# Optimization experiments

Measured on AMD Instinct MI355X. Metric: run time of the kernel, lower is better.

Reference implementation:

```python
import jax, jax.numpy as jnp
import numpy as np

N = 50000      # nodes
E = 800000     # edges (before self-loops)
NFEAT = 128
NHID = 32
H = 8
NCLASS = 47
NEG_SLOPE = 0.2  # PyG GATv2Conv default


def gatv2_layer(x, src, dst, Wl, Wr, att, b, n):
    """One GATv2Conv layer (concat over heads). att: [H, C]."""
    h, c = att.shape
    xl = (x @ Wl).reshape(n, h, c)  # source transform (lin_l)
    xr = (x @ Wr).reshape(n, h, c)  # target transform (lin_r)
    e = jax.nn.leaky_relu(xl[src] + xr[dst], NEG_SLOPE)   # [E, H, C]
    logits = jnp.einsum('ehc,hc->eh', e, att)             # [E, H]
    # segment softmax over incoming edges of each target node
    m = jax.ops.segment_max(logits, dst, num_segments=n)  # [N, H]
    alpha = jnp.exp(logits - m[dst])
    denom = jax.ops.segment_sum(alpha, dst, num_segments=n)
    alpha = alpha / (denom[dst] + 1e-16)
    msg = xl[src] * alpha[:, :, None]                     # [E, H, C]
    out = jax.ops.segment_sum(msg, dst, num_segments=n)   # [N, H, C]
    return out.reshape(n, h * c) + b


def setup_inputs():
    key = jax.random.key(0)
    ks = jax.random.split(key, 16)
    s = 0.1
    x = jax.random.normal(ks[0], (N, NFEAT), jnp.float32)
    edge_index = jax.random.randint(ks[1], (2, E), 0, N)
    HID = H * NHID  # 256
    params = dict(
        Wl0=jax.random.normal(ks[2], (NFEAT, HID), jnp.float32) * s,
        Wr0=jax.random.normal(ks[3], (NFEAT, HID), jnp.float32) * s,
        a0=jax.random.normal(ks[4], (H, NHID), jnp.float32) * s,
        b0=jnp.zeros((HID,), jnp.float32),
        Wl1=jax.random.normal(ks[5], (HID, HID), jnp.float32) * s,
        Wr1=jax.random.normal(ks[6], (HID, HID), jnp.float32) * s,
        a1=jax.random.normal(ks[7], (H, NHID), jnp.float32) * s,
        b1=jnp.zeros((HID,), jnp.float32),
        Wl2=jax.random.normal(ks[8], (HID, NCLASS), jnp.float32) * s,
        Wr2=jax.random.normal(ks[9], (HID, NCLASS), jnp.float32) * s,
        a2=jax.random.normal(ks[10], (1, NCLASS), jnp.float32) * s,
        b2=jnp.zeros((NCLASS,), jnp.float32),
    )
    return {"x": x, "edge_index": edge_index, **params}


def reference(x, edge_index, Wl0, Wr0, a0, b0, Wl1, Wr1, a1, b1, Wl2, Wr2, a2, b2):
    n = x.shape[0]
    # PyG GATv2Conv adds self-loops by default
    loops = jnp.arange(n, dtype=edge_index.dtype)
    src = jnp.concatenate([edge_index[0], loops])
    dst = jnp.concatenate([edge_index[1], loops])
    h = gatv2_layer(x, src, dst, Wl0, Wr0, a0, b0, n)
    h = jax.nn.elu(h)
    h = gatv2_layer(h, src, dst, Wl1, Wr1, a1, b1, n)
    h = jax.nn.elu(h)
    h = gatv2_layer(h, src, dst, Wl2, Wr2, a2, b2, n)
    return jax.nn.log_softmax(h, axis=-1)
```

## Files before the change

kernel.cpp:

```cpp
#include <hip/hip_runtime.h>
#include <cmath>


#define NFEAT 128
#define HID 256
#define NCLS 47
#define L2PAD 64
#define LOG2E 1.44269504088896340736f

typedef __attribute__((ext_vector_type(8))) short bf16x8;
typedef __attribute__((ext_vector_type(4))) float f32x4;
typedef __attribute__((ext_vector_type(2))) float f32x2;

__device__ __forceinline__ unsigned short f2b(float f) {
  unsigned int u = __builtin_bit_cast(unsigned int, f);
  u += 0x7FFFu + ((u >> 16) & 1u);
  return (unsigned short)(u >> 16);
}
__device__ __forceinline__ float b2f(unsigned short s) {
  return __builtin_bit_cast(float, (unsigned int)s << 16);
}
__device__ __forceinline__ f32x2 b2f2(unsigned int u) {
  return (f32x2){__builtin_bit_cast(float, u << 16),
                 __builtin_bit_cast(float, u & 0xFFFF0000u)};
}
__device__ __forceinline__ void glds16(const unsigned short* g, unsigned short* l) {
  __builtin_amdgcn_global_load_lds(
      (const __attribute__((address_space(1))) unsigned int*)g,
      (__attribute__((address_space(3))) unsigned int*)l, 16, 0, 0);
}

__global__ void k_cast_bf16(const float* __restrict__ in,
                            unsigned short* __restrict__ out, int n4) {
  int i = blockIdx.x * blockDim.x + threadIdx.x;
  if (i < n4) {
    float4 v = reinterpret_cast<const float4*>(in)[i];
    ushort4 o = {f2b(v.x), f2b(v.y), f2b(v.z), f2b(v.w)};
    reinterpret_cast<ushort4*>(out)[i] = o;
  }
}

struct WtArgs {
  const float* W[6];
  unsigned short* WT[6];
  int K[6], M[6], off[6], total;
  const float* att;
  float* att48;
};
__global__ void k_wt_all(WtArgs a) {
  int i = blockIdx.x * blockDim.x + threadIdx.x;
  if (i >= a.total) {
    int j = i - a.total;
    if (j < 48) a.att48[j] = (j < NCLS) ? a.att[j] * LOG2E : 0.f;
    return;
  }
  int s = 0;
  #pragma unroll
  for (int j = 1; j < 6; ++j) if (i >= a.off[j]) s = j;
  int jj = i - a.off[s];
  int K = a.K[s], M = a.M[s];
  int m = jj / K, k = jj - m * K;
  a.WT[s][jj] = (m < M) ? f2b(a.W[s][(size_t)k * M + m]) : (unsigned short)0;
}

__global__ void k_init_deg(int* __restrict__ deg, int n) {
  int i = blockIdx.x * blockDim.x + threadIdx.x;
  if (i < n) deg[i] = 1;
}

__global__ void k_count(const int* __restrict__ dst, int* __restrict__ deg, int e) {
  int i = blockIdx.x * blockDim.x + threadIdx.x;
  if (i < e) atomicAdd(&deg[dst[i]], 1);
}

__global__ __launch_bounds__(256) void k_bsum(const int* __restrict__ deg,
                                              int* __restrict__ bsum, int n) {
  int t = threadIdx.x;
  int base = blockIdx.x * 1024 + t * 4;
  int s = 0;
  if (base + 3 < n) {
    int4 v = *reinterpret_cast<const int4*>(deg + base);
    s = v.x + v.y + v.z + v.w;
  } else {
    for (int j = 0; j < 4; ++j) { int i = base + j; if (i < n) s += deg[i]; }
  }
  #pragma unroll
  for (int off = 1; off < 64; off <<= 1) s += __shfl_xor(s, off, 64);
  __shared__ int wsum[4];
  if ((t & 63) == 0) wsum[t >> 6] = s;
  __syncthreads();
  if (t == 0) bsum[blockIdx.x] = wsum[0] + wsum[1] + wsum[2] + wsum[3];
}

__global__ void k_scanb(int* __restrict__ bsum, int nb) {
  int lane = threadIdx.x;
  int v = (lane < nb) ? bsum[lane] : 0;
  #pragma unroll
  for (int off = 1; off < 64; off <<= 1) {
    int u = __shfl_up(v, off, 64);
    if (lane >= off) v += u;
  }
  if (lane < nb) bsum[lane] = v;
}

__global__ __launch_bounds__(256) void k_scanfinal(const int* __restrict__ deg,
                                                   const int* __restrict__ bscan,
                                                   int* __restrict__ rowptr,
                                                   int* __restrict__ adj,
                                                   int* __restrict__ vdst,
                                                   int* __restrict__ cursor, int n) {
  int t = threadIdx.x, b = blockIdx.x;
  int base = b * 1024 + t * 4;
  int v0 = 0, v1 = 0, v2 = 0, v3 = 0;
  if (base + 3 < n) {
    int4 v = *reinterpret_cast<const int4*>(deg + base);
    v0 = v.x; v1 = v.y; v2 = v.z; v3 = v.w;
  } else {
    if (base < n) v0 = deg[base];
    if (base + 1 < n) v1 = deg[base + 1];
    if (base + 2 < n) v2 = deg[base + 2];
    if (base + 3 < n) v3 = deg[base + 3];
  }
  int s = v0 + v1 + v2 + v3;
  int incl = s;
  #pragma unroll
  for (int off = 1; off < 64; off <<= 1) {
    int u = __shfl_up(incl, off, 64);
    if ((t & 63) >= off) incl += u;
  }
  __shared__ int wsum[4];
  int w = t >> 6, l = t & 63;
  if (l == 63) wsum[w] = incl;
  __syncthreads();
  int woff = 0;
  for (int j = 0; j < w; ++j) woff += wsum[j];
  int excl = incl - s + woff;
  int boff = (b == 0) ? 0 : bscan[b - 1];
  int p0 = boff + excl;
  int p1 = p0 + v0, p2 = p1 + v1, p3 = p2 + v2, p4 = p3 + v3;
  if (base < n)     { rowptr[base + 1] = p1; adj[p0] = base;     vdst[p0] = base;     cursor[base]     = p0 + 1; }
  if (base + 1 < n) { rowptr[base + 2] = p2; adj[p1] = base + 1; vdst[p1] = base + 1; cursor[base + 1] = p1 + 1; }
  if (base + 2 < n) { rowptr[base + 3] = p3; adj[p2] = base + 2; vdst[p2] = base + 2; cursor[base + 2] = p2 + 1; }
  if (base + 3 < n) { rowptr[base + 4] = p4; adj[p3] = base + 3; vdst[p3] = base + 3; cursor[base + 3] = p3 + 1; }
  if (b == 0 && t == 0) rowptr[0] = 0;
}

__global__ void k_scatter(const int* __restrict__ src, const int* __restrict__ dst,
                          int* __restrict__ cursor, int* __restrict__ adj,
                          int* __restrict__ vdst, int e) {
  int i = blockIdx.x * blockDim.x + threadIdx.x;
  if (i < e) {
    int d = dst[i];
    int p = atomicAdd(&cursor[d], 1);
    adj[p] = src[i];
    vdst[p] = d;
  }
}

__global__ __launch_bounds__(512) void gemm_dual_bf16_128(
    const unsigned short* __restrict__ X, const unsigned short* __restrict__ WlT,
    const unsigned short* __restrict__ WrT, unsigned short* __restrict__ XL,
    unsigned short* __restrict__ XR, int N, int K, int Mpad) {
  __shared__ __align__(16) unsigned short S[3 * 128 * 64];
  unsigned short* Xs = S;
  unsigned short* Ls = S + 8192;
  unsigned short* Rs = S + 16384;

  const int t = threadIdx.x;
  const int col0 = blockIdx.x * 128;
  const int row0 = blockIdx.y * 128;
  const int w = t >> 6, lane = t & 63;
  const int wr = w >> 2, wc = w & 3;
  const int r15 = lane & 15, kc = lane >> 4;
  const bool tail = (row0 + 128 > N);

  const int row_a = t >> 3,          c16_a = t & 7;
  const int row_b = (t + 512) >> 3,  c16_b = t & 7;
  const int sg_a = (c16_a ^ (row_a & 7)) * 8;
  const int sg_b = (c16_b ^ (row_b & 7)) * 8;
  unsigned short* d0 = S + w * 512;
  unsigned short* d1 = S + 4096 + w * 512;

  f32x4 accL[4][2], accR[4][2];
  #pragma unroll
  for (int rf = 0; rf < 4; ++rf)
    #pragma unroll
    for (int cf = 0; cf < 2; ++cf) {
      accL[rf][cf] = (f32x4){0.f, 0.f, 0.f, 0.f};
      accR[rf][cf] = (f32x4){0.f, 0.f, 0.f, 0.f};
    }

  for (int k0 = 0; k0 < K; k0 += 64) {
    glds16(WlT + (size_t)(col0 + row_a) * K + k0 + sg_a, d0 + 8192);
    glds16(WlT + (size_t)(col0 + row_b) * K + k0 + sg_b, d1 + 8192);
    glds16(WrT + (size_t)(col0 + row_a) * K + k0 + sg_a, d0 + 16384);
    glds16(WrT + (size_t)(col0 + row_b) * K + k0 + sg_b, d1 + 16384);
    if (!tail) {
      glds16(X + (size_t)(row0 + row_a) * K + k0 + sg_a, d0);
      glds16(X + (size_t)(row0 + row_b) * K + k0 + sg_b, d1);
    } else {
      uint4 va = (uint4){0, 0, 0, 0}, vb = (uint4){0, 0, 0, 0};
      if (row0 + row_a < N)
        va = *reinterpret_cast<const uint4*>(X + (size_t)(row0 + row_a) * K + k0 + sg_a);
      if (row0 + row_b < N)
        vb = *reinterpret_cast<const uint4*>(X + (size_t)(row0 + row_b) * K + k0 + sg_b);
      *reinterpret_cast<uint4*>(Xs + row_a * 64 + c16_a * 8) = va;
      *reinterpret_cast<uint4*>(Xs + row_b * 64 + c16_b * 8) = vb;
    }
    __syncthreads();

    #pragma unroll
    for (int ks = 0; ks < 2; ++ks) {
      const int c16 = ks * 4 + kc;
      bf16x8 a[4];
      #pragma unroll
      for (int rf = 0; rf < 4; ++rf) {
        const int rA = wr * 64 + rf * 16 + r15;
        a[rf] = *reinterpret_cast<const bf16x8*>(Xs + rA * 64 + ((c16 ^ (rA & 7)) * 8));
      }
      #pragma unroll
      for (int cf = 0; cf < 2; ++cf) {
        const int rB = wc * 32 + cf * 16 + r15;
        const int so = rB * 64 + ((c16 ^ (rB & 7)) * 8);
        const bf16x8 bl = *reinterpret_cast<const bf16x8*>(Ls + so);
        const bf16x8 br = *reinterpret_cast<const bf16x8*>(Rs + so);
        #pragma unroll
        for (int rf = 0; rf < 4; ++rf) {
          accL[rf][cf] = __builtin_amdgcn_mfma_f32_16x16x32_bf16(a[rf], bl, accL[rf][cf], 0, 0, 0);
          accR[rf][cf] = __builtin_amdgcn_mfma_f32_16x16x32_bf16(a[rf], br, accR[rf][cf], 0, 0, 0);
        }
      }
    }
    __syncthreads();
  }

  #pragma unroll
  for (int rf = 0; rf < 4; ++rf) {
    #pragma unroll
    for (int cf = 0; cf < 2; ++cf) {
      int cc = col0 + wc * 32 + cf * 16 + r15;
      #pragma unroll
      for (int i = 0; i < 4; ++i) {
        int rr = row0 + wr * 64 + rf * 16 + kc * 4 + i;
        if (rr < N) {
          XL[(size_t)rr * Mpad + cc] = f2b(accL[rf][cf][i]);
          XR[(size_t)rr * Mpad + cc] = f2b(accR[rf][cf][i]);
        }
      }
    }
  }
}

__global__ __launch_bounds__(256) void gemm_dual_bf16(
    const unsigned short* __restrict__ X, const unsigned short* __restrict__ WlT,
    const unsigned short* __restrict__ WrT, unsigned short* __restrict__ XL,
    unsigned short* __restrict__ XR, int N, int K, int Mpad) {
  __shared__ __align__(16) unsigned short S[3 * 64 * 64];
  unsigned short* Xs = S;
  unsigned short* Ls = S + 4096;
  unsigned short* Rs = S + 8192;

  const int t = threadIdx.x;
  const int col0 = blockIdx.x * 64;
  const int row0 = blockIdx.y * 64;
  const int w = t >> 6, lane = t & 63;
  const int r15 = lane & 15, kc = lane >> 4;
  const bool tail = (row0 + 64 > N);

  const int rowa = t >> 3, c16a = t & 7;
  const int rowb = (t + 256) >> 3, c16b = t & 7;
  const int sga = (c16a ^ (rowa & 7)) * 8;
  const int sgb = (c16b ^ (rowb & 7)) * 8;
  unsigned short* ldst0 = S + (w * 512);
  unsigned short* ldst1 = S + (2048 + w * 512);

  f32x4 accL[4], accR[4];
  #pragma unroll
  for (int i = 0; i < 4; ++i) {
    accL[i] = (f32x4){0.f, 0.f, 0.f, 0.f};
    accR[i] = (f32x4){0.f, 0.f, 0.f, 0.f};
  }

  const int rA = 16 * w + r15;

  for (int k0 = 0; k0 < K; k0 += 64) {
    glds16(WlT + (size_t)(col0 + rowa) * K + k0 + sga, ldst0 + 4096);
    glds16(WlT + (size_t)(col0 + rowb) * K + k0 + sgb, ldst1 + 4096);
    glds16(WrT + (size_t)(col0 + rowa) * K + k0 + sga, ldst0 + 8192);
    glds16(WrT + (size_t)(col0 + rowb) * K + k0 + sgb, ldst1 + 8192);
    if (!tail) {
      glds16(X + (size_t)(row0 + rowa) * K + k0 + sga, ldst0);
      glds16(X + (size_t)(row0 + rowb) * K + k0 + sgb, ldst1);
    } else {
      uint4 va = (uint4){0, 0, 0, 0}, vb = (uint4){0, 0, 0, 0};
      if (row0 + rowa < N)
        va = *reinterpret_cast<const uint4*>(X + (size_t)(row0 + rowa) * K + k0 + sga);
      if (row0 + rowb < N)
        vb = *reinterpret_cast<const uint4*>(X + (size_t)(row0 + rowb) * K + k0 + sgb);
      *reinterpret_cast<uint4*>(Xs + rowa * 64 + c16a * 8) = va;
      *reinterpret_cast<uint4*>(Xs + rowb * 64 + c16b * 8) = vb;
    }
    __syncthreads();

    #pragma unroll
    for (int ks = 0; ks < 2; ++ks) {
      const int c16 = ks * 4 + kc;
      const bf16x8 a = *reinterpret_cast<const bf16x8*>(
          Xs + rA * 64 + ((c16 ^ (rA & 7)) * 8));
      #pragma unroll
      for (int nf = 0; nf < 4; ++nf) {
        const int rB = nf * 16 + r15;
        const int so = rB * 64 + ((c16 ^ (rB & 7)) * 8);
        const bf16x8 bl = *reinterpret_cast<const bf16x8*>(Ls + so);
        const bf16x8 br = *reinterpret_cast<const bf16x8*>(Rs + so);
        accL[nf] = __builtin_amdgcn_mfma_f32_16x16x32_bf16(a, bl, accL[nf], 0, 0, 0);
        accR[nf] = __builtin_amdgcn_mfma_f32_16x16x32_bf16(a, br, accR[nf], 0, 0, 0);
      }
    }
    __syncthreads();
  }

  #pragma unroll
  for (int nf = 0; nf < 4; ++nf) {
    int cc = col0 + nf * 16 + r15;
    #pragma unroll
    for (int i = 0; i < 4; ++i) {
      int rr = row0 + 16 * w + kc * 4 + i;
      if (rr < N) {
        XL[(size_t)rr * Mpad + cc] = f2b(accL[nf][i]);
        XR[(size_t)rr * Mpad + cc] = f2b(accR[nf][i]);
      }
    }
  }
}

__global__ __launch_bounds__(256) void gat_node_hc(
    const unsigned short* __restrict__ xl, const unsigned short* __restrict__ xr,
    const float* __restrict__ att, const float* __restrict__ bias,
    const int* __restrict__ rowptr, const int* __restrict__ adj,
    unsigned short* __restrict__ out, int n) {
  int wid = (blockIdx.x * blockDim.x + threadIdx.x) >> 6;
  int lane = threadIdx.x & 63;
  if (wid >= n) return;
  const int q = lane & 31, half = lane >> 5;

  const uint4 xrp = *reinterpret_cast<const uint4*>(xr + (size_t)wid * HID + q * 8);
  const f32x2 xr2[4] = {b2f2(xrp.x), b2f2(xrp.y), b2f2(xrp.z), b2f2(xrp.w)};
  const float4 af0 = *reinterpret_cast<const float4*>(att + q * 8);
  const float4 af1 = *reinterpret_cast<const float4*>(att + q * 8 + 4);
  const f32x2 a2[4] = {{af0.x * LOG2E, af0.y * LOG2E}, {af0.z * LOG2E, af0.w * LOG2E},
                       {af1.x * LOG2E, af1.y * LOG2E}, {af1.z * LOG2E, af1.w * LOG2E}};

  float m = -1e30f, denom = 0.f;
  f32x2 acc[4] = {{0.f, 0.f}, {0.f, 0.f}, {0.f, 0.f}, {0.f, 0.f}};

  const int beg = rowptr[wid], end = rowptr[wid + 1];
  for (int base = beg; base < end; base += 2) {
    const int i = base + half;
    const bool act = i < end;
    const int u = adj[act ? i : base];
    const uint4 p = *reinterpret_cast<const uint4*>(xl + (size_t)u * HID + q * 8);
    const f32x2 x2[4] = {b2f2(p.x), b2f2(p.y), b2f2(p.z), b2f2(p.w)};
    f32x2 s2 = {0.f, 0.f};
    #pragma unroll
    for (int j = 0; j < 4; ++j) {
      f32x2 z = x2[j] + xr2[j];
      f32x2 lz = 0.2f * z;
      f32x2 r = {fmaxf(z.x, lz.x), fmaxf(z.y, lz.y)};
      s2 += r * a2[j];
    }
    float part = s2.x + s2.y;
    part += __shfl_xor(part, 1, 64);
    part += __shfl_xor(part, 2, 64);
    if (!act) part = -1e30f;
    if (__any(part > m + 11.54f)) {
      float mn = fmaxf(m, part);
      float so = exp2f(m - mn);
      float wn = act ? exp2f(part - mn) : 0.f;
      denom = denom * so + wn;
      #pragma unroll
      for (int j = 0; j < 4; ++j) acc[j] = acc[j] * so + wn * x2[j];
      m = mn;
    } else {
      float wn = act ? exp2f(part - m) : 0.f;
      denom += wn;
      #pragma unroll
      for (int j = 0; j < 4; ++j) acc[j] += wn * x2[j];
    }
  }

  float mo = __shfl_xor(m, 32, 64);
  float ms = fmaxf(m, mo);
  float sc = exp2f(m - ms);
  denom *= sc;
  denom += __shfl_xor(denom, 32, 64);
  #pragma unroll
  for (int j = 0; j < 4; ++j) {
    acc[j] *= sc;
    acc[j].x += __shfl_xor(acc[j].x, 32, 64);
    acc[j].y += __shfl_xor(acc[j].y, 32, 64);
  }

  if (half == 0) {
    const float inv = 1.f / (denom + 1e-16f);
    const float4 bf0 = *reinterpret_cast<const float4*>(bias + q * 8);
    const float4 bf1 = *reinterpret_cast<const float4*>(bias + q * 8 + 4);
    float o[8] = {acc[0].x * inv + bf0.x, acc[0].y * inv + bf0.y,
                  acc[1].x * inv + bf0.z, acc[1].y * inv + bf0.w,
                  acc[2].x * inv + bf1.x, acc[2].y * inv + bf1.y,
                  acc[3].x * inv + bf1.z, acc[3].y * inv + bf1.w};
    #pragma unroll
    for (int j = 0; j < 8; ++j) o[j] = o[j] > 0.f ? o[j] : (__expf(o[j]) - 1.f);
    uint4 ov;
    ov.x = (unsigned)f2b(o[0]) | ((unsigned)f2b(o[1]) << 16);
    ov.y = (unsigned)f2b(o[2]) | ((unsigned)f2b(o[3]) << 16);
    ov.z = (unsigned)f2b(o[4]) | ((unsigned)f2b(o[5]) << 16);
    ov.w = (unsigned)f2b(o[6]) | ((unsigned)f2b(o[7]) << 16);
    *reinterpret_cast<uint4*>(out + (size_t)wid * HID + q * 8) = ov;
  }
}

__global__ __launch_bounds__(256) void k_logit_l2(
    const unsigned short* __restrict__ xl, const unsigned short* __restrict__ xr,
    const float* __restrict__ att48, const int* __restrict__ adj,
    const int* __restrict__ vdst, float* __restrict__ logit, int total) {
  int i = blockIdx.x * blockDim.x + threadIdx.x;
  if (i >= total) return;
  const int u = adj[i], v = vdst[i];
  const uint4* pu = reinterpret_cast<const uint4*>(xl + (size_t)u * L2PAD);
  const uint4* pv = reinterpret_cast<const uint4*>(xr + (size_t)v * L2PAD);
  f32x2 s2 = {0.f, 0.f};
  #pragma unroll
  for (int b = 0; b < 6; ++b) {
    const uint4 xu = pu[b], xv = pv[b];
    const f32x2* a2 = reinterpret_cast<const f32x2*>(att48 + b * 8);
    const unsigned ua[4] = {xu.x, xu.y, xu.z, xu.w};
    const unsigned va[4] = {xv.x, xv.y, xv.z, xv.w};
    #pragma unroll
    for (int j = 0; j < 4; ++j) {
      f32x2 z = b2f2(ua[j]) + b2f2(va[j]);
      f32x2 lz = 0.2f * z;
      f32x2 r = {fmaxf(z.x, lz.x), fmaxf(z.y, lz.y)};
      s2 += r * a2[j];
    }
  }
  logit[i] = s2.x + s2.y;
}

__global__ __launch_bounds__(256) void gat_node_l2(
    const unsigned short* __restrict__ xl, const float* __restrict__ logit,
    const float* __restrict__ bias, const int* __restrict__ rowptr,
    const int* __restrict__ adj, float* __restrict__ out, int n) {
  int wid = (blockIdx.x * blockDim.x + threadIdx.x) >> 6;
  int lane = threadIdx.x & 63;
  if (wid >= n) return;
  const bool act = lane < NCLS;
  const int beg = rowptr[wid], end = rowptr[wid + 1];

  float mx = -1e30f;
  for (int i = beg + lane; i < end; i += 64) mx = fmaxf(mx, logit[i]);
  #pragma unroll
  for (int off = 1; off < 64; off <<= 1) mx = fmaxf(mx, __shfl_xor(mx, off, 64));

  float denom = 0.f, acc = 0.f;
  int i = beg;
  for (; i + 1 < end; i += 2) {
    int u0 = adj[i], u1 = adj[i + 1];
    float w0 = exp2f(logit[i] - mx);
    float w1 = exp2f(logit[i + 1] - mx);
    float x0 = act ? b2f(xl[(size_t)u0 * L2PAD + lane]) : 0.f;
    float x1 = act ? b2f(xl[(size_t)u1 * L2PAD + lane]) : 0.f;
    denom += w0 + w1;
    acc += w0 * x0 + w1 * x1;
  }
  if (i < end) {
    int u0 = adj[i];
    float w0 = exp2f(logit[i] - mx);
    float x0 = act ? b2f(xl[(size_t)u0 * L2PAD + lane]) : 0.f;
    denom += w0;
    acc += w0 * x0;
  }

  float r = acc / (denom + 1e-16f) + (act ? bias[lane] : 0.f);
  float rm = act ? r : -1e30f;
  #pragma unroll
  for (int off = 1; off < 64; off <<= 1) rm = fmaxf(rm, __shfl_xor(rm, off, 64));
  float se = act ? __expf(r - rm) : 0.f;
  #pragma unroll
  for (int off = 1; off < 64; off <<= 1) se += __shfl_xor(se, off, 64);
  if (act) out[(size_t)wid * NCLS + lane] = r - rm - __logf(se);
}

extern "C" void kernel_launch(void* const* d_in, const int* in_sizes, int n_in,
                              void* d_out, int out_size, void* d_ws, size_t ws_size,
                              hipStream_t stream) {
  const float* x   = (const float*)d_in[0];
  const int* ei    = (const int*)d_in[1];
  const float* Wl0 = (const float*)d_in[2];
  const float* Wr0 = (const float*)d_in[3];
  const float* a0  = (const float*)d_in[4];
  const float* b0  = (const float*)d_in[5];
  const float* Wl1 = (const float*)d_in[6];
  const float* Wr1 = (const float*)d_in[7];
  const float* a1  = (const float*)d_in[8];
  const float* b1  = (const float*)d_in[9];
  const float* Wl2 = (const float*)d_in[10];
  const float* Wr2 = (const float*)d_in[11];
  const float* a2  = (const float*)d_in[12];
  const float* b2  = (const float*)d_in[13];

  const int N = in_sizes[0] / NFEAT;
  const int E = in_sizes[1] / 2;
  const int* src = ei;
  const int* dst = ei + E;
  const int total = E + N;

  char* ws = (char*)d_ws;
  unsigned short* xlb = (unsigned short*)ws; ws += (size_t)N * HID * 2;
  unsigned short* xrb = (unsigned short*)ws; ws += (size_t)N * HID * 2;
  unsigned short* xb  = (unsigned short*)ws; ws += (size_t)N * HID * 2;
  unsigned short* hb  = (unsigned short*)ws; ws += (size_t)N * HID * 2;
  unsigned short* WT  = (unsigned short*)ws; ws += (size_t)6 * HID * HID * 2;
  float* logit = (float*)ws; ws += (size_t)total * sizeof(float);
  float* att48 = (float*)ws; ws += 64 * sizeof(float);
  int* deg    = (int*)ws; ws += (size_t)N * sizeof(int);
  int* rowptr = (int*)ws; ws += (size_t)(N + 8) * sizeof(int);
  int* bsum   = (int*)ws; ws += (size_t)64 * sizeof(int);
  int* adj    = (int*)ws; ws += (size_t)total * sizeof(int);
  int* vdst   = (int*)ws; ws += (size_t)total * sizeof(int);

  unsigned short* WlT0 = WT + 0 * HID * HID;
  unsigned short* WrT0 = WT + 1 * HID * HID;
  unsigned short* WlT1 = WT + 2 * HID * HID;
  unsigned short* WrT1 = WT + 3 * HID * HID;
  unsigned short* WlT2 = WT + 4 * HID * HID;
  unsigned short* WrT2 = WT + 5 * HID * HID;

  const int TB = 256;
  const int nbScan = (N + 1023) / 1024;

  k_cast_bf16<<<(N * NFEAT / 4 + TB - 1) / TB, TB, 0, stream>>>(x, xb, N * NFEAT / 4);
  {
    WtArgs a;
    const float* Wsrc[6] = {Wl0, Wr0, Wl1, Wr1, Wl2, Wr2};
    unsigned short* Wdst[6] = {WlT0, WrT0, WlT1, WrT1, WlT2, WrT2};
    int Ks[6] = {NFEAT, NFEAT, HID, HID, HID, HID};
    int Ms[6] = {HID, HID, HID, HID, NCLS, NCLS};
    int Mp[6] = {HID, HID, HID, HID, L2PAD, L2PAD};
    int off = 0;
    for (int s = 0; s < 6; ++s) {
      a.W[s] = Wsrc[s]; a.WT[s] = Wdst[s]; a.K[s] = Ks[s]; a.M[s] = Ms[s];
      a.off[s] = off; off += Mp[s] * Ks[s];
    }
    a.total = off;
    a.att = a2; a.att48 = att48;
    k_wt_all<<<(a.total + 48 + TB - 1) / TB, TB, 0, stream>>>(a);
  }

  k_init_deg<<<(N + TB - 1) / TB, TB, 0, stream>>>(deg, N);
  k_count<<<(E + TB - 1) / TB, TB, 0, stream>>>(dst, deg, E);
  k_bsum<<<nbScan, TB, 0, stream>>>(deg, bsum, N);
  k_scanb<<<1, 64, 0, stream>>>(bsum, nbScan);
  k_scanfinal<<<nbScan, TB, 0, stream>>>(deg, bsum, rowptr, adj, vdst, deg, N);
  k_scatter<<<(E + TB - 1) / TB, TB, 0, stream>>>(src, dst, deg, adj, vdst, E);

  const int nodeBlocks = (N + 3) / 4;
  const int rb128 = (N + 127) / 128;
  const int rb64 = (N + 63) / 64;

  {
    dim3 g(HID / 128, rb128);
    gemm_dual_bf16_128<<<g, 512, 0, stream>>>(xb, WlT0, WrT0, xlb, xrb, N, NFEAT, HID);
    gat_node_hc<<<nodeBlocks, 256, 0, stream>>>(xlb, xrb, a0, b0, rowptr, adj, hb, N);
  }
  {
    dim3 g(HID / 128, rb128);
    gemm_dual_bf16_128<<<g, 512, 0, stream>>>(hb, WlT1, WrT1, xlb, xrb, N, HID, HID);
    gat_node_hc<<<nodeBlocks, 256, 0, stream>>>(xlb, xrb, a1, b1, rowptr, adj, xb, N);
  }
  {
    dim3 g(1, rb64);
    gemm_dual_bf16<<<g, 256, 0, stream>>>(xb, WlT2, WrT2, xlb, xrb, N, HID, L2PAD);
    k_logit_l2<<<(total + TB - 1) / TB, TB, 0, stream>>>(xlb, xrb, att48, adj,
                                                         vdst, logit, total);
    gat_node_l2<<<nodeBlocks, 256, 0, stream>>>(xlb, logit, b2, rowptr, adj,
                                                (float*)d_out, N);
  }
}
```

Measured before the change: 431.9 us.

## Fuse init kernels, precompute layer-2 segment max via atomics, use DPP reductions

Folds the degree initialisation and a new per-node max buffer reset into the cast kernel, removing one launch. The layer-2 logit kernel now records each destination's maximum logit with an order-preserving integer atomicMax, so the node kernel no longer makes a separate pass over the logits to find it. In the layer-0/1 attention kernel the quad reduction uses DPP moves instead of shuffles, exp2 with LOG2E prescaling becomes __expf, and the rescale threshold drops from 11.54 to 8. The change adds about 850k atomics on the node-max buffer and slightly alters the numerics of the online softmax.

```diff
diff --git a/kernel.cpp b/kernel.cpp
--- a/kernel.cpp
+++ b/kernel.cpp
@@ -30,13 +30,37 @@
       (__attribute__((address_space(3))) unsigned int*)l, 16, 0, 0);
 }
 
+__device__ __forceinline__ float quad_sum(float v) {
+  int t = __builtin_amdgcn_mov_dpp(__builtin_bit_cast(int, v), 0xB1, 0xF, 0xF, true);
+  v += __builtin_bit_cast(float, t);
+  t = __builtin_amdgcn_mov_dpp(__builtin_bit_cast(int, v), 0x4E, 0xF, 0xF, true);
+  v += __builtin_bit_cast(float, t);
+  return v;
+}
+
+__device__ __forceinline__ unsigned fenc(float f) {
+  unsigned b = __builtin_bit_cast(unsigned, f);
+  return b ^ (((int)b >> 31) | 0x80000000u);
+}
+__device__ __forceinline__ float fdec(unsigned e) {
+  unsigned b = (e & 0x80000000u) ? (e ^ 0x80000000u) : ~e;
+  return __builtin_bit_cast(float, b);
+}
+
 __global__ void k_cast_bf16(const float* __restrict__ in,
-                            unsigned short* __restrict__ out, int n4) {
+                            unsigned short* __restrict__ out, int n4,
+                            int* __restrict__ deg, unsigned* __restrict__ nmx,
+                            int n) {
   int i = blockIdx.x * blockDim.x + threadIdx.x;
   if (i < n4) {
     float4 v = reinterpret_cast<const float4*>(in)[i];
     ushort4 o = {f2b(v.x), f2b(v.y), f2b(v.z), f2b(v.w)};
     reinterpret_cast<ushort4*>(out)[i] = o;
+  } else if (i < n4 + n) {
+    deg[i - n4] = 1;
+  } else {
+    int j = i - n4 - n;
+    if (j < n) nmx[j] = 0u;
   }
 }
 
@@ -61,11 +85,6 @@
   int K = a.K[s], M = a.M[s];
   int m = jj / K, k = jj - m * K;
   a.WT[s][jj] = (m < M) ? f2b(a.W[s][(size_t)k * M + m]) : (unsigned short)0;
-}
-
-__global__ void k_init_deg(int* __restrict__ deg, int n) {
-  int i = blockIdx.x * blockDim.x + threadIdx.x;
-  if (i < n) deg[i] = 1;
 }
 
 __global__ void k_count(const int* __restrict__ dst, int* __restrict__ deg, int e) {
@@ -348,8 +367,8 @@
   const f32x2 xr2[4] = {b2f2(xrp.x), b2f2(xrp.y), b2f2(xrp.z), b2f2(xrp.w)};
   const float4 af0 = *reinterpret_cast<const float4*>(att + q * 8);
   const float4 af1 = *reinterpret_cast<const float4*>(att + q * 8 + 4);
-  const f32x2 a2[4] = {{af0.x * LOG2E, af0.y * LOG2E}, {af0.z * LOG2E, af0.w * LOG2E},
-                       {af1.x * LOG2E, af1.y * LOG2E}, {af1.z * LOG2E, af1.w * LOG2E}};
+  const f32x2 a2[4] = {{af0.x, af0.y}, {af0.z, af0.w},
+                       {af1.x, af1.y}, {af1.z, af1.w}};
 
   float m = -1e30f, denom = 0.f;
   f32x2 acc[4] = {{0.f, 0.f}, {0.f, 0.f}, {0.f, 0.f}, {0.f, 0.f}};
@@ -369,20 +388,18 @@
       f32x2 r = {fmaxf(z.x, lz.x), fmaxf(z.y, lz.y)};
       s2 += r * a2[j];
     }
-    float part = s2.x + s2.y;
-    part += __shfl_xor(part, 1, 64);
-    part += __shfl_xor(part, 2, 64);
+    float part = quad_sum(s2.x + s2.y);
     if (!act) part = -1e30f;
-    if (__any(part > m + 11.54f)) {
+    if (__any(part > m + 8.f)) {
       float mn = fmaxf(m, part);
-      float so = exp2f(m - mn);
-      float wn = act ? exp2f(part - mn) : 0.f;
+      float so = __expf(m - mn);
+      float wn = act ? __expf(part - mn) : 0.f;
       denom = denom * so + wn;
       #pragma unroll
       for (int j = 0; j < 4; ++j) acc[j] = acc[j] * so + wn * x2[j];
       m = mn;
     } else {
-      float wn = act ? exp2f(part - m) : 0.f;
+      float wn = act ? __expf(part - m) : 0.f;
       denom += wn;
       #pragma unroll
       for (int j = 0; j < 4; ++j) acc[j] += wn * x2[j];
@@ -391,7 +408,7 @@
 
   float mo = __shfl_xor(m, 32, 64);
   float ms = fmaxf(m, mo);
-  float sc = exp2f(m - ms);
+  float sc = __expf(m - ms);
   denom *= sc;
   denom += __shfl_xor(denom, 32, 64);
   #pragma unroll
@@ -423,7 +440,8 @@
 __global__ __launch_bounds__(256) void k_logit_l2(
     const unsigned short* __restrict__ xl, const unsigned short* __restrict__ xr,
     const float* __restrict__ att48, const int* __restrict__ adj,
-    const int* __restrict__ vdst, float* __restrict__ logit, int total) {
+    const int* __restrict__ vdst, float* __restrict__ logit,
+    unsigned* __restrict__ nmx, int total) {
   int i = blockIdx.x * blockDim.x + threadIdx.x;
   if (i >= total) return;
   const int u = adj[i], v = vdst[i];
@@ -444,23 +462,23 @@
       s2 += r * a2[j];
     }
   }
-  logit[i] = s2.x + s2.y;
+  float lg = s2.x + s2.y;
+  logit[i] = lg;
+  atomicMax(&nmx[v], fenc(lg));
 }
 
 __global__ __launch_bounds__(256) void gat_node_l2(
     const unsigned short* __restrict__ xl, const float* __restrict__ logit,
     const float* __restrict__ bias, const int* __restrict__ rowptr,
-    const int* __restrict__ adj, float* __restrict__ out, int n) {
+    const int* __restrict__ adj, const unsigned* __restrict__ nmx,
+    float* __restrict__ out, int n) {
   int wid = (blockIdx.x * blockDim.x + threadIdx.x) >> 6;
   int lane = threadIdx.x & 63;
   if (wid >= n) return;
   const bool act = lane < NCLS;
   const int beg = rowptr[wid], end = rowptr[wid + 1];
 
-  float mx = -1e30f;
-  for (int i = beg + lane; i < end; i += 64) mx = fmaxf(mx, logit[i]);
-  #pragma unroll
-  for (int off = 1; off < 64; off <<= 1) mx = fmaxf(mx, __shfl_xor(mx, off, 64));
+  const float mx = fdec(nmx[wid]);
 
   float denom = 0.f, acc = 0.f;
   int i = beg;
@@ -523,6 +541,7 @@
   unsigned short* WT  = (unsigned short*)ws; ws += (size_t)6 * HID * HID * 2;
   float* logit = (float*)ws; ws += (size_t)total * sizeof(float);
   float* att48 = (float*)ws; ws += 64 * sizeof(float);
+  unsigned* nmx = (unsigned*)ws; ws += (size_t)N * sizeof(unsigned);
   int* deg    = (int*)ws; ws += (size_t)N * sizeof(int);
   int* rowptr = (int*)ws; ws += (size_t)(N + 8) * sizeof(int);
   int* bsum   = (int*)ws; ws += (size_t)64 * sizeof(int);
@@ -538,8 +557,9 @@
 
   const int TB = 256;
   const int nbScan = (N + 1023) / 1024;
-
-  k_cast_bf16<<<(N * NFEAT / 4 + TB - 1) / TB, TB, 0, stream>>>(x, xb, N * NFEAT / 4);
+  const int n4 = N * NFEAT / 4;
+
+  k_cast_bf16<<<(n4 + 2 * N + TB - 1) / TB, TB, 0, stream>>>(x, xb, n4, deg, nmx, N);
   {
     WtArgs a;
     const float* Wsrc[6] = {Wl0, Wr0, Wl1, Wr1, Wl2, Wr2};
@@ -557,7 +577,6 @@
     k_wt_all<<<(a.total + 48 + TB - 1) / TB, TB, 0, stream>>>(a);
   }
 
-  k_init_deg<<<(N + TB - 1) / TB, TB, 0, stream>>>(deg, N);
   k_count<<<(E + TB - 1) / TB, TB, 0, stream>>>(dst, deg, E);
   k_bsum<<<nbScan, TB, 0, stream>>>(deg, bsum, N);
   k_scanb<<<1, 64, 0, stream>>>(bsum, nbScan);
@@ -582,8 +601,8 @@
     dim3 g(1, rb64);
     gemm_dual_bf16<<<g, 256, 0, stream>>>(xb, WlT2, WrT2, xlb, xrb, N, HID, L2PAD);
     k_logit_l2<<<(total + TB - 1) / TB, TB, 0, stream>>>(xlb, xrb, att48, adj,
-                                                         vdst, logit, total);
-    gat_node_l2<<<nodeBlocks, 256, 0, stream>>>(xlb, logit, b2, rowptr, adj,
+                                                         vdst, logit, nmx, total);
+    gat_node_l2<<<nodeBlocks, 256, 0, stream>>>(xlb, logit, b2, rowptr, adj, nmx,
                                                 (float*)d_out, N);
   }
 }
```

Result: slower. 452.3 us (+4.7%).
